# Kernel tuning notes

Measured on AMD Instinct MI355X. Metric: run time of the kernel, lower is better.

## Reference

```python
import jax, jax.numpy as jnp
import numpy as np

BLANK_ID = 0
B, MAX_T, MAX_U, VOCAB = 4, 200, 101, 1024  # MAX_U = max_label_len + 1


def setup_inputs() -> dict:
    key = jax.random.key(0)
    k1, k2, k3 = jax.random.split(key, 3)
    logits = jax.random.normal(k1, (B, MAX_T, MAX_U, VOCAB), dtype=jnp.float32)
    labels = jax.random.randint(k2, (B, MAX_U - 1), 0, VOCAB).astype(jnp.int64)
    label_lengths = jax.random.randint(k3, (B,), 1, MAX_U).astype(jnp.int64)  # in [1, MAX_U-1]
    attention_mask = jnp.ones((B, MAX_T), dtype=jnp.int32)
    return {"logits": logits, "labels": labels,
            "label_lengths": label_lengths, "attention_mask": attention_mask}


def _alpha_lattice(blank_lp, label_lp):
    """Forward variables for one sample.

    blank_lp: [T, U]   log P(blank | t, u)
    label_lp: [T, U-1] log P(y_u | t, u)  (label emitted at grid column u)
    Returns alpha [T, U], matching the reference recursion:
      alpha[0,0]   = blank_lp[0,0]
      alpha[t,0]   = alpha[t-1,0] + blank_lp[t,0]
      alpha[0,u]   = alpha[0,u-1] + label_lp[0,u-1]
      alpha[t,u]   = logaddexp(alpha[t-1,u]+blank_lp[t,u], alpha[t,u-1]+label_lp[t,u-1])
    """
    # First row: pure label path (cumulative sum along u).
    row0 = blank_lp[0, 0] + jnp.concatenate(
        [jnp.zeros((1,), blank_lp.dtype), jnp.cumsum(label_lp[0])])

    def time_step(prev_row, xs):
        b_t, l_t = xs                 # [U], [U-1]
        from_blank = prev_row + b_t   # blank transition into row t

        def u_step(carry, x):
            bl, lb = x
            a = jnp.logaddexp(bl, carry + lb)
            return a, a

        _, rest = jax.lax.scan(u_step, from_blank[0], (from_blank[1:], l_t))
        row = jnp.concatenate([from_blank[:1], rest])
        return row, row

    _, rows = jax.lax.scan(time_step, row0, (blank_lp[1:], label_lp[1:]))
    return jnp.concatenate([row0[None], rows], axis=0)  # [T, U]


def reference(logits, labels, label_lengths, attention_mask):
    Bn, maxT, maxU, V = logits.shape
    input_lengths = jnp.clip(attention_mask.sum(axis=1).astype(jnp.int32), 1, maxT)
    lab_lens = jnp.clip(label_lengths.astype(jnp.int32), 0, maxU - 1)
    labels_c = jnp.clip(labels, 0, V - 1)

    lp = jax.nn.log_softmax(logits, axis=-1)          # [B, T, U, V]
    blank_lp = lp[..., BLANK_ID]                      # [B, T, U]
    # label_lp[b, t, u] = lp[b, t, u, labels[b, u]] for u in [0, U-2]
    idx = jnp.broadcast_to(labels_c[:, None, :, None], (Bn, maxT, maxU - 1, 1))
    label_lp = jnp.take_along_axis(lp[:, :, :-1, :], idx, axis=3)[..., 0]

    alpha = jax.vmap(_alpha_lattice)(blank_lp, label_lp)  # [B, T, U]

    t_idx = input_lengths - 1
    u_idx = lab_lens                                  # U_b - 1 = label_len
    loss_b = -alpha[jnp.arange(Bn), t_idx, u_idx]

    valid = (input_lengths > 0) & (lab_lens > 0)
    loss_b = jnp.where(valid, loss_b, 0.0)
    num_valid = jnp.maximum(valid.sum(), 1)
    return loss_b.sum() / num_valid                   # reduction='mean'
```

## Files before the change

kernel.cpp:

```cpp
#include <hip/hip_runtime.h>
#include <hip/hip_bf16.h>
#include <math.h>

#define BB 4
#define TT 200
#define UU 101
#define VV 1024
#define NCELL (BB*TT*UU)

#define DSTRIDE 102
#define BROWS 300
#define LROWS 301

__device__ __forceinline__ float f4max(const float4& v) {
    return fmaxf(fmaxf(v.x, v.y), fmaxf(v.z, v.w));
}
__device__ __forceinline__ float f4comp(const float4& v, int c) {
    switch (c & 3) { case 0: return v.x; case 1: return v.y; case 2: return v.z; default: return v.w; }
}

__global__ __launch_bounds__(256) void lse_kernel(
        const float* __restrict__ logits,
        const int*   __restrict__ labels,
        float* __restrict__ blankD,
        float* __restrict__ labD) {
    const int wave = threadIdx.x >> 6;
    const int lane = threadIdx.x & 63;
    const int cell = blockIdx.x * 4 + wave;
    if (cell >= NCELL) return;
    const int b   = cell / (TT * UU);
    const int rem = cell % (TT * UU);
    const int t   = rem / UU;
    const int u   = rem % UU;

    const float4* src = (const float4*)(logits + (size_t)cell * VV);
    float4 x0 = src[lane];
    float4 x1 = src[lane + 64];
    float4 x2 = src[lane + 128];
    float4 x3 = src[lane + 192];

    float m = fmaxf(fmaxf(f4max(x0), f4max(x1)), fmaxf(f4max(x2), f4max(x3)));
    #pragma unroll
    for (int off = 32; off; off >>= 1) m = fmaxf(m, __shfl_xor(m, off));

    float s = 0.f;
    s += __expf(x0.x - m) + __expf(x0.y - m) + __expf(x0.z - m) + __expf(x0.w - m);
    s += __expf(x1.x - m) + __expf(x1.y - m) + __expf(x1.z - m) + __expf(x1.w - m);
    s += __expf(x2.x - m) + __expf(x2.y - m) + __expf(x2.z - m) + __expf(x2.w - m);
    s += __expf(x3.x - m) + __expf(x3.y - m) + __expf(x3.z - m) + __expf(x3.w - m);
    #pragma unroll
    for (int off = 32; off; off >>= 1) s += __shfl_xor(s, off);

    const float lse = m + __logf(s);

    if (lane == 0)
        blankD[(size_t)b * BROWS * DSTRIDE + (t + u) * DSTRIDE + u] = x0.x - lse;

    if (u < UU - 1) {
        int l = labels[b * (UU - 1) + u];
        l = min(max(l, 0), VV - 1);
        const int lane_l = (l >> 2) & 63;
        if (lane == lane_l) {
            const int j = l >> 8;
            const int c = l & 3;
            float val = (j == 0) ? f4comp(x0, c) : (j == 1) ? f4comp(x1, c)
                      : (j == 2) ? f4comp(x2, c) : f4comp(x3, c);
            labD[(size_t)b * LROWS * DSTRIDE + (t + u + 1) * DSTRIDE + (u + 1)] = val - lse;
        }
    }
}

__global__ __launch_bounds__(64) void alpha_kernel(
        const float* __restrict__ blankD,
        const float* __restrict__ labD,
        const int*   __restrict__ lab_lens,
        const int*   __restrict__ attn,
        float* __restrict__ loss_b,
        int*   __restrict__ valid_b) {
    const int b = blockIdx.x;
    const int lane = threadIdx.x;

    __shared__ float s_loss;
    if (lane == 0) s_loss = 0.f;

    int acc = 0;
    for (int i = lane; i < TT; i += 64) acc += attn[b * TT + i];
    #pragma unroll
    for (int off = 32; off; off >>= 1) acc += __shfl_xor(acc, off);
    const int inlen = min(max(acc, 1), TT);
    const int tmax = inlen - 1;
    int lab = lab_lens[b];
    lab = min(max(lab, 0), UU - 1);
    const int ndiag = tmax + lab + 1;

    const float* blb = blankD + (size_t)b * BROWS * DSTRIDE;
    const float* llb = labD   + (size_t)b * LROWS * DSTRIDE;

    const int c0 = 2 * lane;
    const int c1 = 2 * lane + 1;
    const int cc = min(c0, 100);

    auto loadB = [&](int d) -> float2 {
        return *(const float2*)(blb + min(d, BROWS - 1) * DSTRIDE + cc);
    };
    auto loadL = [&](int d) -> float2 {
        return *(const float2*)(llb + min(d, LROWS - 1) * DSTRIDE + cc);
    };

    constexpr int Q = 4;
    float2 qb[Q], ql[Q];
    #pragma unroll
    for (int k = 0; k < Q; ++k) { qb[k] = loadB(k); ql[k] = loadL(k); }

    float prevA = 0.f, prevB = 0.f;

    for (int d = 0; d < ndiag; ++d) {
        const int slot = d & (Q - 1);
        const float2 bl = qb[slot];
        const float2 lb = ql[slot];
        qb[slot] = loadB(d + Q);
        ql[slot] = loadL(d + Q);

        const float upB = __shfl_up(prevB, 1);

        float newA;
        if (lane == 0) {
            newA = (d == 0) ? bl.x : prevA + bl.x;
        } else if (d == c0) {
            newA = upB + lb.x;
        } else {
            const float a = prevA + bl.x;
            const float c = upB + lb.x;
            const float mx = fmaxf(a, c), mn = fminf(a, c);
            newA = mx + __logf(1.f + __expf(mn - mx));
        }

        float newB;
        if (d == c1) {
            newB = prevA + lb.y;
        } else {
            const float a = prevB + bl.y;
            const float c = prevA + lb.y;
            const float mx = fmaxf(a, c), mn = fminf(a, c);
            newB = mx + __logf(1.f + __expf(mn - mx));
        }

        if (d == ndiag - 1) {
            if (c0 == lab) s_loss = -newA;
            if (c1 == lab) s_loss = -newB;
        }
        prevA = newA;
        prevB = newB;
    }

    __syncthreads();
    if (lane == 0) {
        loss_b[b]  = s_loss;
        valid_b[b] = (lab > 0) ? 1 : 0;
    }
}

__global__ void finalize_kernel(const float* __restrict__ loss_b,
                                const int* __restrict__ valid_b,
                                float* __restrict__ out) {
    if (threadIdx.x == 0 && blockIdx.x == 0) {
        float s = 0.f;
        int nv = 0;
        for (int b = 0; b < BB; ++b) {
            if (valid_b[b]) { s += loss_b[b]; ++nv; }
        }
        out[0] = s / (float)max(nv, 1);
    }
}

extern "C" void kernel_launch(void* const* d_in, const int* in_sizes, int n_in,
                              void* d_out, int out_size, void* d_ws, size_t ws_size,
                              hipStream_t stream) {
    const float* logits   = (const float*)d_in[0];
    const int*   labels   = (const int*)d_in[1];
    const int*   lab_lens = (const int*)d_in[2];
    const int*   attn     = (const int*)d_in[3];

    float* ws      = (float*)d_ws;
    float* blankD  = ws;
    float* labD    = blankD + BB * BROWS * DSTRIDE;
    float* loss_b  = labD   + BB * LROWS * DSTRIDE;
    int*   valid_b = (int*)(loss_b + BB);

    lse_kernel<<<(NCELL + 3) / 4, 256, 0, stream>>>(logits, labels, blankD, labD);
    alpha_kernel<<<BB, 64, 0, stream>>>(blankD, labD, lab_lens, attn, loss_b, valid_b);
    finalize_kernel<<<1, 64, 0, stream>>>(loss_b, valid_b, (float*)d_out);
}
```

Baseline: 577.9 us.

## Fuse finalize into single-block alpha kernel and use nontemporal logit loads

```diff
diff --git a/kernel.cpp b/kernel.cpp
--- a/kernel.cpp
+++ b/kernel.cpp
@@ -12,10 +12,12 @@
 #define BROWS 300
 #define LROWS 301
 
-__device__ __forceinline__ float f4max(const float4& v) {
+typedef float vfloat4 __attribute__((ext_vector_type(4)));
+
+__device__ __forceinline__ float v4max(const vfloat4& v) {
     return fmaxf(fmaxf(v.x, v.y), fmaxf(v.z, v.w));
 }
-__device__ __forceinline__ float f4comp(const float4& v, int c) {
+__device__ __forceinline__ float v4comp(const vfloat4& v, int c) {
     switch (c & 3) { case 0: return v.x; case 1: return v.y; case 2: return v.z; default: return v.w; }
 }
 
@@ -33,13 +35,13 @@
     const int t   = rem / UU;
     const int u   = rem % UU;
 
-    const float4* src = (const float4*)(logits + (size_t)cell * VV);
-    float4 x0 = src[lane];
-    float4 x1 = src[lane + 64];
-    float4 x2 = src[lane + 128];
-    float4 x3 = src[lane + 192];
+    const vfloat4* src = (const vfloat4*)(logits + (size_t)cell * VV);
+    vfloat4 x0 = __builtin_nontemporal_load(src + lane);
+    vfloat4 x1 = __builtin_nontemporal_load(src + lane + 64);
+    vfloat4 x2 = __builtin_nontemporal_load(src + lane + 128);
+    vfloat4 x3 = __builtin_nontemporal_load(src + lane + 192);
 
-    float m = fmaxf(fmaxf(f4max(x0), f4max(x1)), fmaxf(f4max(x2), f4max(x3)));
+    float m = fmaxf(fmaxf(v4max(x0), v4max(x1)), fmaxf(v4max(x2), v4max(x3)));
     #pragma unroll
     for (int off = 32; off; off >>= 1) m = fmaxf(m, __shfl_xor(m, off));
 
@@ -63,25 +65,24 @@
         if (lane == lane_l) {
             const int j = l >> 8;
             const int c = l & 3;
-            float val = (j == 0) ? f4comp(x0, c) : (j == 1) ? f4comp(x1, c)
-                      : (j == 2) ? f4comp(x2, c) : f4comp(x3, c);
+            float val = (j == 0) ? v4comp(x0, c) : (j == 1) ? v4comp(x1, c)
+                      : (j == 2) ? v4comp(x2, c) : v4comp(x3, c);
             labD[(size_t)b * LROWS * DSTRIDE + (t + u + 1) * DSTRIDE + (u + 1)] = val - lse;
         }
     }
 }
 
-__global__ __launch_bounds__(64) void alpha_kernel(
+__global__ __launch_bounds__(256) void alpha_kernel(
         const float* __restrict__ blankD,
         const float* __restrict__ labD,
         const int*   __restrict__ lab_lens,
         const int*   __restrict__ attn,
-        float* __restrict__ loss_b,
-        int*   __restrict__ valid_b) {
-    const int b = blockIdx.x;
-    const int lane = threadIdx.x;
+        float* __restrict__ out) {
+    const int b    = threadIdx.x >> 6;
+    const int lane = threadIdx.x & 63;
 
-    __shared__ float s_loss;
-    if (lane == 0) s_loss = 0.f;
+    __shared__ float s_loss[BB];
+    __shared__ int   s_lab[BB];
 
     int acc = 0;
     for (int i = lane; i < TT; i += 64) acc += attn[b * TT + i];
@@ -91,6 +92,7 @@
     const int tmax = inlen - 1;
     int lab = lab_lens[b];
     lab = min(max(lab, 0), UU - 1);
+    if (lane == 0) s_lab[b] = lab;
     const int ndiag = tmax + lab + 1;
 
     const float* blb = blankD + (size_t)b * BROWS * DSTRIDE;
@@ -107,7 +109,7 @@
         return *(const float2*)(llb + min(d, LROWS - 1) * DSTRIDE + cc);
     };
 
-    constexpr int Q = 4;
+    constexpr int Q = 8;
     float2 qb[Q], ql[Q];
     #pragma unroll
     for (int k = 0; k < Q; ++k) { qb[k] = loadB(k); ql[k] = loadL(k); }
@@ -123,6 +125,16 @@
 
         const float upB = __shfl_up(prevB, 1);
 
+        float newB;
+        if (d == c1) {
+            newB = prevA + lb.y;
+        } else {
+            const float a = prevB + bl.y;
+            const float c = prevA + lb.y;
+            const float mx = fmaxf(a, c), mn = fminf(a, c);
+            newB = mx + __logf(1.f + __expf(mn - mx));
+        }
+
         float newA;
         if (lane == 0) {
             newA = (d == 0) ? bl.x : prevA + bl.x;
@@ -135,39 +147,21 @@
             newA = mx + __logf(1.f + __expf(mn - mx));
         }
 
-        float newB;
-        if (d == c1) {
-            newB = prevA + lb.y;
-        } else {
-            const float a = prevB + bl.y;
-            const float c = prevA + lb.y;
-            const float mx = fmaxf(a, c), mn = fminf(a, c);
-            newB = mx + __logf(1.f + __expf(mn - mx));
-        }
-
         if (d == ndiag - 1) {
-            if (c0 == lab) s_loss = -newA;
-            if (c1 == lab) s_loss = -newB;
+            if (c0 == lab) s_loss[b] = -newA;
+            if (c1 == lab) s_loss[b] = -newB;
         }
         prevA = newA;
         prevB = newB;
     }
 
     __syncthreads();
-    if (lane == 0) {
-        loss_b[b]  = s_loss;
-        valid_b[b] = (lab > 0) ? 1 : 0;
-    }
-}
-
-__global__ void finalize_kernel(const float* __restrict__ loss_b,
-                                const int* __restrict__ valid_b,
-                                float* __restrict__ out) {
-    if (threadIdx.x == 0 && blockIdx.x == 0) {
+    if (threadIdx.x == 0) {
         float s = 0.f;
         int nv = 0;
-        for (int b = 0; b < BB; ++b) {
-            if (valid_b[b]) { s += loss_b[b]; ++nv; }
+        #pragma unroll
+        for (int i = 0; i < BB; ++i) {
+            if (s_lab[i] > 0) { s += s_loss[i]; ++nv; }
         }
         out[0] = s / (float)max(nv, 1);
     }
@@ -184,10 +178,7 @@
     float* ws      = (float*)d_ws;
     float* blankD  = ws;
     float* labD    = blankD + BB * BROWS * DSTRIDE;
-    float* loss_b  = labD   + BB * LROWS * DSTRIDE;
-    int*   valid_b = (int*)(loss_b + BB);
 
     lse_kernel<<<(NCELL + 3) / 4, 256, 0, stream>>>(logits, labels, blankD, labD);
-    alpha_kernel<<<BB, 64, 0, stream>>>(blankD, labD, lab_lens, attn, loss_b, valid_b);
-    finalize_kernel<<<1, 64, 0, stream>>>(loss_b, valid_b, (float*)d_out);
+    alpha_kernel<<<1, 256, 0, stream>>>(blankD, labD, lab_lens, attn, (float*)d_out);
 }
```

After: 565.8 us. 2.1% less time.
